# Performance work log

Hardware: AMD Instinct MI355X
Metric: run time of the kernel (lower is better)

The kernel has to match this reference:

```python
import jax, jax.numpy as jnp
import numpy as np

B, D, T = 256, 128, 512
E, H, WH, WIN = 128, 512, 512, 64

def setup_inputs() -> dict:
    key = jax.random.key(0)
    ks = jax.random.split(key, 13)
    def rn(k, shape, scale=0.05):
        return jax.random.normal(k, shape, dtype=jnp.float32) * scale
    return {
        "z_ctx": rn(ks[0], (B, D, WIN), 1.0),
        "z": rn(ks[1], (B, D, T), 1.0),
        "z_slow": rn(ks[2], (B, D, T), 1.0),
        "z_fast": rn(ks[3], (B, D, T), 1.0),
        "e": rn(ks[4], (B, E), 1.0),
        "W_enc": rn(ks[5], (WH, D * WIN)),
        "b_enc": rn(ks[6], (WH,)),
        "W_ih": rn(ks[7], (3 * H, WH + E)),
        "W_hh": rn(ks[8], (3 * H, H)),
        "b_ih": rn(ks[9], (3 * H,)),
        "b_hh": rn(ks[10], (3 * H,)),
        "W_fc": rn(ks[11], (D, H)),
        "b_fc": rn(ks[12], (D,)),
    }

def reference(z_ctx, z, z_slow, z_fast, e, W_enc, b_enc, W_ih, W_hh, b_ih, b_hh, W_fc, b_fc):
    # teacher_forcing=False path (deterministic reference)
    Bb, Dd, Tt = z.shape
    # SlowWindowEncoder: flatten window + Linear + ReLU -> [B, WH]
    context = jax.nn.relu(z_ctx.reshape(Bb, -1) @ W_enc.T + b_enc)
    slow_input = jnp.concatenate([context, e], axis=-1)  # constant over t
    gi = slow_input @ W_ih.T + b_ih                      # [B, 3H], precomputed
    i_r, i_z, i_n = jnp.split(gi, 3, axis=-1)
    Hh = W_hh.shape[1]
    h0 = jnp.zeros((Bb, Hh), dtype=z.dtype)
    zp0 = z_ctx[:, :, -1]                                # z_slow_prev init

    def step(carry, _):
        h, zp = carry
        gh = h @ W_hh.T + b_hh
        h_r, h_z, h_n = jnp.split(gh, 3, axis=-1)
        r = jax.nn.sigmoid(i_r + h_r)
        zg = jax.nn.sigmoid(i_z + h_z)
        n = jnp.tanh(i_n + r * h_n)
        h_new = (1.0 - zg) * n + zg * h                  # GRUCell update
        zh = zp + h_new @ W_fc.T + b_fc                  # residual delta
        return (h_new, zh), zh

    _, zs = jax.lax.scan(step, (h0, zp0), None, length=Tt)  # [T, B, D]
    return jnp.transpose(zs, (1, 2, 0))                  # [B, D, T]
```

## Files before the change

kernel.cpp:

```cpp
#include <hip/hip_runtime.h>

typedef __attribute__((ext_vector_type(8))) short s8v;
typedef __attribute__((ext_vector_type(4))) float f4v;
typedef __attribute__((ext_vector_type(4))) unsigned int u4v;

#define MFMA16(a, b, c) __builtin_amdgcn_mfma_f32_16x16x32_bf16((a), (b), (c), 0, 0, 0)

__device__ __forceinline__ unsigned short f2bf(float f) {
  unsigned u = __float_as_uint(f);
  return (unsigned short)((u + 0x7fffu + ((u >> 16) & 1u)) >> 16);
}

__global__ void cvt4_kernel(const float* __restrict__ in, unsigned short* __restrict__ out, int n4) {
  int i = blockIdx.x * blockDim.x + threadIdx.x;
  if (i >= n4) return;
  float4 v = ((const float4*)in)[i];
  ushort4 o;
  o.x = f2bf(v.x); o.y = f2bf(v.y); o.z = f2bf(v.z); o.w = f2bf(v.w);
  ((ushort4*)out)[i] = o;
}

__global__ void build_slow_kernel(const float* __restrict__ context, const float* __restrict__ e,
                                  unsigned short* __restrict__ out) {
  int i = blockIdx.x * blockDim.x + threadIdx.x;
  if (i >= 256 * 640) return;
  int b = i / 640, c = i - b * 640;
  float v = (c < 512) ? context[b * 512 + c] : e[b * 128 + (c - 512)];
  out[i] = f2bf(v);
}

template <int RELU>
__global__ __launch_bounds__(256) void gemm_bt(const unsigned short* __restrict__ A,
                                               const unsigned short* __restrict__ B,
                                               const float* __restrict__ bias, float* __restrict__ C,
                                               int M, int N, int K) {
  __shared__ unsigned short As[64][48];
  __shared__ unsigned short Bs[64][48];
  int tid = threadIdx.x;
  int lane = tid & 63, w = tid >> 6;
  int m = lane & 15, q = lane >> 4;
  int row0 = blockIdx.x * 64, col0 = blockIdx.y * 64;
  int sr = tid >> 2, sk = (tid & 3) * 8;
  const unsigned short* Ap = A + (size_t)(row0 + sr) * K + sk;
  const unsigned short* Bp = B + (size_t)(col0 + sr) * K + sk;
  f4v acc[4];
#pragma unroll
  for (int nt = 0; nt < 4; nt++) acc[nt] = (f4v){0.f, 0.f, 0.f, 0.f};

  for (int k0 = 0; k0 < K; k0 += 32) {
    *(uint4*)&As[sr][sk] = *(const uint4*)(Ap + k0);
    *(uint4*)&Bs[sr][sk] = *(const uint4*)(Bp + k0);
    __syncthreads();
    s8v a = *(const s8v*)&As[w * 16 + m][q * 8];
#pragma unroll
    for (int nt = 0; nt < 4; nt++) {
      s8v bb = *(const s8v*)&Bs[nt * 16 + m][q * 8];
      acc[nt] = MFMA16(a, bb, acc[nt]);
    }
    __syncthreads();
  }
#pragma unroll
  for (int nt = 0; nt < 4; nt++) {
    int c = col0 + nt * 16 + m;
    float bv = bias[c];
#pragma unroll
    for (int i = 0; i < 4; i++) {
      int r = row0 + w * 16 + q * 4 + i;
      float v = acc[nt][i] + bv;
      if (RELU) v = v > 0.f ? v : 0.f;
      C[(size_t)r * N + c] = v;
    }
  }
}

__global__ __launch_bounds__(64) void gru_scan6(const float* __restrict__ gi,
                                                const unsigned short* __restrict__ Whh,
                                                const float* __restrict__ bhh,
                                                unsigned long long* __restrict__ Hall8,
                                                unsigned int* __restrict__ flags) {
  __shared__ unsigned short wlds[6 * 16 * 64 * 8];
  int tid = threadIdx.x;
  int bid = blockIdx.x;
  int bg = bid >> 4, cg = bid & 15;
  int b0 = bg * 16;
  int n = tid & 15, q = tid >> 4;

#pragma unroll 1
  for (int it = 0; it < 96; ++it) {
    int g = it >> 5, rem = it & 31, ct = rem >> 4, kc = rem & 15;
    int row = g * 512 + cg * 32 + ct * 16 + n;
    const unsigned short* wb = Whh + (size_t)row * 512 + kc * 32;
    unsigned short* dst = &wlds[(((g * 2 + ct) * 16 + kc) * 64 + tid) * 8];
    *(uint2*)dst = *(const uint2*)(wb + q * 4);
    *(uint2*)(dst + 4) = *(const uint2*)(wb + 16 + q * 4);
  }

  float gir[2][4], giz[2][4], gin[2][4], bhn[2][4];
#pragma unroll
  for (int ct = 0; ct < 2; ++ct) {
#pragma unroll
    for (int i = 0; i < 4; ++i) {
      int c = cg * 32 + ct * 16 + q * 4 + i;
      const float* gp = gi + (size_t)(b0 + n) * 1536 + c;
      gir[ct][i] = gp[0] + bhh[c];
      giz[ct][i] = gp[512] + bhh[c + 512];
      gin[ct][i] = gp[1024];
      bhn[ct][i] = bhh[c + 1024];
    }
  }
  float hp[2][4] = {{0.f, 0.f, 0.f, 0.f}, {0.f, 0.f, 0.f, 0.f}};
  __syncthreads();

  unsigned int* myflag = flags + bg * 32 + cg;
  const unsigned int* pollp = flags + bg * 32 + (tid & 3) * 4;
  size_t rowbase = (size_t)(b0 + n) * 512 * 128;

#pragma unroll 1
  for (int t = 0; t < 512; ++t) {
    f4v ar[2], az[2], an[2];
#pragma unroll
    for (int ct = 0; ct < 2; ++ct) {
      ar[ct] = (f4v){gir[ct][0], gir[ct][1], gir[ct][2], gir[ct][3]};
      az[ct] = (f4v){giz[ct][0], giz[ct][1], giz[ct][2], giz[ct][3]};
      an[ct] = (f4v){bhn[ct][0], bhn[ct][1], bhn[ct][2], bhn[ct][3]};
    }
    if (t > 0) {
      unsigned tgt = (unsigned)t;
      for (long sp = 0; sp < 500000L; ++sp) {
        unsigned m0 = tgt, m1 = tgt, m2 = tgt, m3 = tgt;
        if (tid < 4) {
          u4v fv;
          asm volatile("global_load_dwordx4 %0, %1, off sc0 sc1\n\ts_waitcnt vmcnt(0)"
                       : "=v"(fv)
                       : "v"(pollp)
                       : "memory");
          m0 = fv[0]; m1 = fv[1]; m2 = fv[2]; m3 = fv[3];
        }
        bool ok = (m0 >= tgt) && (m1 >= tgt) && (m2 >= tgt) && (m3 >= tgt);
        if (__ballot(ok) == 0xffffffffffffffffULL) break;
        if ((sp & 63) == 63) __builtin_amdgcn_fence(__ATOMIC_ACQUIRE, "agent");
      }
      asm volatile("" ::: "memory");
      const char* hb = (const char*)(Hall8 + rowbase + (size_t)(t - 1) * 128) + q * 16;
      s8v bf[16];
#pragma unroll
      for (int kc = 0; kc < 16; ++kc) {
        asm volatile("global_load_dwordx4 %0, %1, off sc0 sc1"
                     : "=v"(bf[kc])
                     : "v"(hb + (size_t)kc * 64)
                     : "memory");
      }
      asm volatile("s_waitcnt vmcnt(0)" ::: "memory");
      __builtin_amdgcn_sched_barrier(0);
#pragma unroll
      for (int kc = 0; kc < 16; ++kc) {
#pragma unroll
        for (int ct = 0; ct < 2; ++ct) {
          s8v a0 = *(const s8v*)&wlds[(((0 + ct) * 16 + kc) * 64 + tid) * 8];
          ar[ct] = MFMA16(a0, bf[kc], ar[ct]);
          s8v a1 = *(const s8v*)&wlds[(((2 + ct) * 16 + kc) * 64 + tid) * 8];
          az[ct] = MFMA16(a1, bf[kc], az[ct]);
          s8v a2 = *(const s8v*)&wlds[(((4 + ct) * 16 + kc) * 64 + tid) * 8];
          an[ct] = MFMA16(a2, bf[kc], an[ct]);
        }
      }
    }
    unsigned long long hu[2];
#pragma unroll
    for (int ct = 0; ct < 2; ++ct) {
      union { unsigned short s[4]; unsigned long long u; } pk;
#pragma unroll
      for (int i = 0; i < 4; ++i) {
        float r = 1.f / (1.f + __expf(-ar[ct][i]));
        float zg = 1.f / (1.f + __expf(-az[ct][i]));
        float x = gin[ct][i] + r * an[ct][i];
        float ex = __expf(2.f * x);
        float nn = 1.f - 2.f / (ex + 1.f);
        float h = (1.f - zg) * nn + zg * hp[ct][i];
        hp[ct][i] = h;
        pk.s[i] = f2bf(h);
      }
      hu[ct] = pk.u;
    }
    {
      u4v stv;
      stv[0] = (unsigned)hu[0];
      stv[1] = (unsigned)(hu[0] >> 32);
      stv[2] = (unsigned)hu[1];
      stv[3] = (unsigned)(hu[1] >> 32);
      unsigned long long* hstp = Hall8 + rowbase + (size_t)t * 128 + (size_t)(cg * 8 + q * 2);
      asm volatile("global_store_dwordx4 %0, %1, off sc0 sc1" ::"v"(hstp), "v"(stv) : "memory");
    }
    asm volatile("s_waitcnt vmcnt(0)" ::: "memory");
    if (tid == 0) {
      unsigned fv = (unsigned)(t + 1);
      asm volatile("global_store_dword %0, %1, off sc0 sc1" ::"v"(myflag), "v"(fv) : "memory");
    }
  }
}

__global__ __launch_bounds__(256) void fc_scan(const unsigned short* __restrict__ Hall,
                                               const unsigned short* __restrict__ Wfc,
                                               const float* __restrict__ bfc,
                                               const float* __restrict__ zctx,
                                               float* __restrict__ out) {
  __shared__ unsigned short hs[16][520];
  int tid = threadIdx.x;
  int lane = tid & 63, w = tid >> 6;
  int m = lane & 15, q = lane >> 4;
  int b = blockIdx.x;

  s8v wf[2][16];
  float bf_r[2], carry[2];
#pragma unroll
  for (int j = 0; j < 2; j++) {
    int d = (2 * w + j) * 16 + m;
#pragma unroll
    for (int kc = 0; kc < 16; kc++) {
      const unsigned short* wb = Wfc + (size_t)d * 512 + kc * 32;
      union { uint2 u2[2]; s8v v; } wu;
      wu.u2[0] = *(const uint2*)(wb + q * 4);
      wu.u2[1] = *(const uint2*)(wb + 16 + q * 4);
      wf[j][kc] = wu.v;
    }
    bf_r[j] = bfc[d];
    carry[j] = zctx[((size_t)b * 128 + d) * 64 + 63];
  }

#pragma unroll 1
  for (int chunk = 0; chunk < 32; chunk++) {
    int t0 = chunk * 16;
    {
      int mm = tid >> 4, ci = (tid & 15) * 4;
      const unsigned short* src = Hall + ((size_t)b * 512 + t0 + mm) * 512 + ci * 8;
#pragma unroll
      for (int o = 0; o < 4; o++) {
        uint4 v = *(const uint4*)(src + o * 8);
        *(uint4*)&hs[mm][(ci + o) * 8] = v;
      }
    }
    __syncthreads();
    s8v af[16];
#pragma unroll
    for (int kc = 0; kc < 16; kc++) af[kc] = *(const s8v*)&hs[m][kc * 32 + q * 8];
    f4v acc[2];
    acc[0] = (f4v){0.f, 0.f, 0.f, 0.f};
    acc[1] = (f4v){0.f, 0.f, 0.f, 0.f};
#pragma unroll
    for (int kc = 0; kc < 16; kc++) {
      acc[0] = MFMA16(af[kc], wf[0][kc], acc[0]);
      acc[1] = MFMA16(af[kc], wf[1][kc], acc[1]);
    }
    __syncthreads();

#pragma unroll
    for (int j = 0; j < 2; j++) {
      float s0 = acc[j][0] + bf_r[j];
      float s1 = s0 + acc[j][1] + bf_r[j];
      float s2 = s1 + acc[j][2] + bf_r[j];
      float s3 = s2 + acc[j][3] + bf_r[j];
      float tot = s3;
      float incl = tot;
      float u = __shfl_up(incl, 16, 64);
      if (q >= 1) incl += u;
      u = __shfl_up(incl, 32, 64);
      if (q >= 2) incl += u;
      float excl = incl - tot;
      float add = excl + carry[j];
      int d = (2 * w + j) * 16 + m;
      float4 o4 = make_float4(s0 + add, s1 + add, s2 + add, s3 + add);
      *(float4*)(out + ((size_t)b * 128 + d) * 512 + t0 + q * 4) = o4;
      float chunktot = __shfl(incl, 48 + m, 64);
      carry[j] += chunktot;
    }
  }
}

extern "C" void kernel_launch(void* const* d_in, const int* in_sizes, int n_in,
                              void* d_out, int out_size, void* d_ws, size_t ws_size,
                              hipStream_t stream) {
  const float* z_ctx = (const float*)d_in[0];
  const float* e     = (const float*)d_in[4];
  const float* W_enc = (const float*)d_in[5];
  const float* b_enc = (const float*)d_in[6];
  const float* W_ih  = (const float*)d_in[7];
  const float* W_hh  = (const float*)d_in[8];
  const float* b_ih  = (const float*)d_in[9];
  const float* b_hh  = (const float*)d_in[10];
  const float* W_fc  = (const float*)d_in[11];
  const float* b_fc  = (const float*)d_in[12];
  float* out = (float*)d_out;

  char* ws = (char*)d_ws;
  const size_t OFF_WENC = 0;
  const size_t OFF_ZCTX = 8388608;
  const size_t OFF_WIH  = 12582912;
  const size_t OFF_WHH  = 14548992;
  const size_t OFF_WFC  = 16121856;
  const size_t OFF_CTX  = 16252928;
  const size_t OFF_SLOW = 16777216;
  const size_t OFF_GI   = 17104896;
  const size_t OFF_HALL = 18677760;
  const size_t OFF_SYNC = OFF_HALL + 134217728ull;
  const size_t NEED = OFF_SYNC + 32768;
  if (ws_size < NEED) return;

  unsigned short* Wenc_bf = (unsigned short*)(ws + OFF_WENC);
  unsigned short* zctx_bf = (unsigned short*)(ws + OFF_ZCTX);
  unsigned short* Wih_bf  = (unsigned short*)(ws + OFF_WIH);
  unsigned short* Whh_bf  = (unsigned short*)(ws + OFF_WHH);
  unsigned short* Wfc_bf  = (unsigned short*)(ws + OFF_WFC);
  float* context          = (float*)(ws + OFF_CTX);
  unsigned short* slow_bf = (unsigned short*)(ws + OFF_SLOW);
  float* gi               = (float*)(ws + OFF_GI);
  unsigned short* Hall    = (unsigned short*)(ws + OFF_HALL);
  unsigned long long* Hall8 = (unsigned long long*)(ws + OFF_HALL);
  unsigned int* flags     = (unsigned int*)(ws + OFF_SYNC);

  hipMemsetAsync(flags, 0, 4096, stream);

  cvt4_kernel<<<4096, 256, 0, stream>>>(W_enc, Wenc_bf, 512 * 8192 / 4);
  cvt4_kernel<<<2048, 256, 0, stream>>>(z_ctx, zctx_bf, 256 * 8192 / 4);
  cvt4_kernel<<<960, 256, 0, stream>>>(W_ih, Wih_bf, 1536 * 640 / 4);
  cvt4_kernel<<<768, 256, 0, stream>>>(W_hh, Whh_bf, 1536 * 512 / 4);
  cvt4_kernel<<<64, 256, 0, stream>>>(W_fc, Wfc_bf, 128 * 512 / 4);

  gemm_bt<1><<<dim3(4, 8), 256, 0, stream>>>(zctx_bf, Wenc_bf, b_enc, context, 256, 512, 8192);
  build_slow_kernel<<<640, 256, 0, stream>>>(context, e, slow_bf);
  gemm_bt<0><<<dim3(4, 24), 256, 0, stream>>>(slow_bf, Wih_bf, b_ih, gi, 256, 1536, 640);

  {
    const float* gi_c = gi;
    const unsigned short* whh_c = Whh_bf;
    const float* bhh_c = b_hh;
    unsigned long long* hall_c = Hall8;
    unsigned int* flags_c = flags;
    void* args[] = {(void*)&gi_c, (void*)&whh_c, (void*)&bhh_c, (void*)&hall_c, (void*)&flags_c};
    hipError_t err = hipLaunchCooperativeKernel((void*)gru_scan6, dim3(256), dim3(64), args, 0, stream);
    if (err != hipSuccess) {
      gru_scan6<<<256, 64, 0, stream>>>(gi, Whh_bf, b_hh, Hall8, flags);
    }
  }

  fc_scan<<<256, 256, 0, stream>>>(Hall, Wfc_bf, b_fc, z_ctx, out);
}
```

Before: 2.660 ms.

## Replace flag-based inter-block sync with sentinel polling on hidden-state data

Removes per-step flag stores and flag polling in the GRU scan. Instead the hidden-state buffer is pre-filled with 0xFF, and consumers spin-load the previous step's h directly until no sentinel words remain. This cuts one dependent global round-trip and the store-then-flag wait from each of the 512 serial steps. It adds a large memset of the hidden-state buffer and relies on valid bf16 pairs never equalling the sentinel pattern.

```diff
diff --git a/kernel.cpp b/kernel.cpp
--- a/kernel.cpp
+++ b/kernel.cpp
@@ -73,11 +73,10 @@
   }
 }
 
-__global__ __launch_bounds__(64) void gru_scan6(const float* __restrict__ gi,
+__global__ __launch_bounds__(64) void gru_scan8(const float* __restrict__ gi,
                                                 const unsigned short* __restrict__ Whh,
                                                 const float* __restrict__ bhh,
-                                                unsigned long long* __restrict__ Hall8,
-                                                unsigned int* __restrict__ flags) {
+                                                unsigned long long* __restrict__ Hall8) {
   __shared__ unsigned short wlds[6 * 16 * 64 * 8];
   int tid = threadIdx.x;
   int bid = blockIdx.x;
@@ -111,8 +110,6 @@
   float hp[2][4] = {{0.f, 0.f, 0.f, 0.f}, {0.f, 0.f, 0.f, 0.f}};
   __syncthreads();
 
-  unsigned int* myflag = flags + bg * 32 + cg;
-  const unsigned int* pollp = flags + bg * 32 + (tid & 3) * 4;
   size_t rowbase = (size_t)(b0 + n) * 512 * 128;
 
 #pragma unroll 1
@@ -125,43 +122,39 @@
       an[ct] = (f4v){bhn[ct][0], bhn[ct][1], bhn[ct][2], bhn[ct][3]};
     }
     if (t > 0) {
-      unsigned tgt = (unsigned)t;
+      const char* hb = (const char*)(Hall8 + rowbase + (size_t)(t - 1) * 128) + q * 16;
+      u4v bfu[16];
       for (long sp = 0; sp < 500000L; ++sp) {
-        unsigned m0 = tgt, m1 = tgt, m2 = tgt, m3 = tgt;
-        if (tid < 4) {
-          u4v fv;
-          asm volatile("global_load_dwordx4 %0, %1, off sc0 sc1\n\ts_waitcnt vmcnt(0)"
-                       : "=v"(fv)
-                       : "v"(pollp)
+#pragma unroll
+        for (int kc = 0; kc < 16; ++kc) {
+          asm volatile("global_load_dwordx4 %0, %1, off sc0 sc1"
+                       : "=v"(bfu[kc])
+                       : "v"(hb + (size_t)kc * 64)
                        : "memory");
-          m0 = fv[0]; m1 = fv[1]; m2 = fv[2]; m3 = fv[3];
         }
-        bool ok = (m0 >= tgt) && (m1 >= tgt) && (m2 >= tgt) && (m3 >= tgt);
+        asm volatile("s_waitcnt vmcnt(0)" ::: "memory");
+        bool ok = true;
+#pragma unroll
+        for (int kc = 0; kc < 16; ++kc) {
+          ok = ok && (bfu[kc][0] != 0xFFFFFFFFu) && (bfu[kc][1] != 0xFFFFFFFFu) &&
+               (bfu[kc][2] != 0xFFFFFFFFu) && (bfu[kc][3] != 0xFFFFFFFFu);
+        }
         if (__ballot(ok) == 0xffffffffffffffffULL) break;
-        if ((sp & 63) == 63) __builtin_amdgcn_fence(__ATOMIC_ACQUIRE, "agent");
+        if ((sp & 255) == 255) __builtin_amdgcn_fence(__ATOMIC_ACQUIRE, "agent");
       }
-      asm volatile("" ::: "memory");
-      const char* hb = (const char*)(Hall8 + rowbase + (size_t)(t - 1) * 128) + q * 16;
-      s8v bf[16];
+      __builtin_amdgcn_sched_barrier(0);
 #pragma unroll
       for (int kc = 0; kc < 16; ++kc) {
-        asm volatile("global_load_dwordx4 %0, %1, off sc0 sc1"
-                     : "=v"(bf[kc])
-                     : "v"(hb + (size_t)kc * 64)
-                     : "memory");
-      }
-      asm volatile("s_waitcnt vmcnt(0)" ::: "memory");
-      __builtin_amdgcn_sched_barrier(0);
-#pragma unroll
-      for (int kc = 0; kc < 16; ++kc) {
+        union { u4v u; s8v s; } bb;
+        bb.u = bfu[kc];
 #pragma unroll
         for (int ct = 0; ct < 2; ++ct) {
           s8v a0 = *(const s8v*)&wlds[(((0 + ct) * 16 + kc) * 64 + tid) * 8];
-          ar[ct] = MFMA16(a0, bf[kc], ar[ct]);
+          ar[ct] = MFMA16(a0, bb.s, ar[ct]);
           s8v a1 = *(const s8v*)&wlds[(((2 + ct) * 16 + kc) * 64 + tid) * 8];
-          az[ct] = MFMA16(a1, bf[kc], az[ct]);
+          az[ct] = MFMA16(a1, bb.s, az[ct]);
           s8v a2 = *(const s8v*)&wlds[(((4 + ct) * 16 + kc) * 64 + tid) * 8];
-          an[ct] = MFMA16(a2, bf[kc], an[ct]);
+          an[ct] = MFMA16(a2, bb.s, an[ct]);
         }
       }
     }
@@ -190,11 +183,6 @@
       stv[3] = (unsigned)(hu[1] >> 32);
       unsigned long long* hstp = Hall8 + rowbase + (size_t)t * 128 + (size_t)(cg * 8 + q * 2);
       asm volatile("global_store_dwordx4 %0, %1, off sc0 sc1" ::"v"(hstp), "v"(stv) : "memory");
-    }
-    asm volatile("s_waitcnt vmcnt(0)" ::: "memory");
-    if (tid == 0) {
-      unsigned fv = (unsigned)(t + 1);
-      asm volatile("global_store_dword %0, %1, off sc0 sc1" ::"v"(myflag), "v"(fv) : "memory");
     }
   }
 }
@@ -301,8 +289,8 @@
   const size_t OFF_SLOW = 16777216;
   const size_t OFF_GI   = 17104896;
   const size_t OFF_HALL = 18677760;
-  const size_t OFF_SYNC = OFF_HALL + 134217728ull;
-  const size_t NEED = OFF_SYNC + 32768;
+  const size_t HALL_SZ  = 134217728ull;
+  const size_t NEED = OFF_HALL + HALL_SZ + 32768;
   if (ws_size < NEED) return;
 
   unsigned short* Wenc_bf = (unsigned short*)(ws + OFF_WENC);
@@ -315,9 +303,8 @@
   float* gi               = (float*)(ws + OFF_GI);
   unsigned short* Hall    = (unsigned short*)(ws + OFF_HALL);
   unsigned long long* Hall8 = (unsigned long long*)(ws + OFF_HALL);
-  unsigned int* flags     = (unsigned int*)(ws + OFF_SYNC);
-
-  hipMemsetAsync(flags, 0, 4096, stream);
+
+  (void)hipMemsetAsync(Hall, 0xFF, HALL_SZ, stream);
 
   cvt4_kernel<<<4096, 256, 0, stream>>>(W_enc, Wenc_bf, 512 * 8192 / 4);
   cvt4_kernel<<<2048, 256, 0, stream>>>(z_ctx, zctx_bf, 256 * 8192 / 4);
@@ -334,11 +321,10 @@
     const unsigned short* whh_c = Whh_bf;
     const float* bhh_c = b_hh;
     unsigned long long* hall_c = Hall8;
-    unsigned int* flags_c = flags;
-    void* args[] = {(void*)&gi_c, (void*)&whh_c, (void*)&bhh_c, (void*)&hall_c, (void*)&flags_c};
-    hipError_t err = hipLaunchCooperativeKernel((void*)gru_scan6, dim3(256), dim3(64), args, 0, stream);
+    void* args[] = {(void*)&gi_c, (void*)&whh_c, (void*)&bhh_c, (void*)&hall_c};
+    hipError_t err = hipLaunchCooperativeKernel((void*)gru_scan8, dim3(256), dim3(64), args, 0, stream);
     if (err != hipSuccess) {
-      gru_scan6<<<256, 64, 0, stream>>>(gi, Whh_bf, b_hh, Hall8, flags);
+      gru_scan8<<<256, 64, 0, stream>>>(gi, Whh_bf, b_hh, Hall8);
     }
   }
 
```

Measured after the change: 2.994 ms. 12.5% more time.
